# Kernel optimization log

Hardware: AMD Instinct MI355X
Metric: run time of the kernel (lower is better)

Reference implementation:

```python
import jax, jax.numpy as jnp
import numpy as np

B, C, L = 8, 2048, 256          # batch, seq (EEG channels), feature length
E = 3 * L                        # embed_dim = 768 (fused QKV width)
H = 4                            # attention heads
D = E // (3 * H)                 # head_dim = 64
SCALE = 8.0                      # hardcoded in the module (== sqrt(D) here)


def _layer_norm(x, gamma, beta, eps=1e-5):
    mu = jnp.mean(x, axis=-1, keepdims=True)
    var = jnp.var(x, axis=-1, keepdims=True)
    return (x - mu) * jax.lax.rsqrt(var + eps) * gamma + beta


def setup_inputs() -> dict:
    key = jax.random.key(0)
    ks = jax.random.split(key, 5)
    x = jax.random.normal(ks[0], (B, C, L), dtype=jnp.float32)
    # layers_1: Linear(L -> E) + LayerNorm(E)
    W1 = jax.random.normal(ks[1], (L, E), dtype=jnp.float32) / np.sqrt(L)
    b1 = jnp.zeros((E,), dtype=jnp.float32)
    g1 = jnp.ones((E,), dtype=jnp.float32)
    beta1 = jnp.zeros((E,), dtype=jnp.float32)
    # layers_2: Linear(L -> L) + LayerNorm(L)
    W2 = jax.random.normal(ks[2], (L, L), dtype=jnp.float32) / np.sqrt(L)
    b2 = jnp.zeros((L,), dtype=jnp.float32)
    g2 = jnp.ones((L,), dtype=jnp.float32)
    beta2 = jnp.zeros((L,), dtype=jnp.float32)
    return {"x": x, "W1": W1, "b1": b1, "g1": g1, "beta1": beta1,
            "W2": W2, "b2": b2, "g2": g2, "beta2": beta2}


def reference(x, W1, b1, g1, beta1, W2, b2, g2, beta2):
    b, c, _ = x.shape
    # layers_1 (dropout is identity in eval mode)
    y = _layer_norm(x @ W1 + b1, g1, beta1)                     # [b, c, E]
    qkv = y.reshape(b, c, 3, H, D).transpose(2, 0, 3, 1, 4)     # [3, b, H, c, D]
    q, k, v = qkv[0], qkv[1], qkv[2]
    attn = jax.nn.softmax(jnp.einsum('bhqd,bhkd->bhqk', q, k) / SCALE, axis=-1)
    o = jnp.einsum('bhqk,bhkd->bhqd', attn, v)                  # [b, H, c, D]
    o = o.transpose(0, 2, 1, 3).reshape(b, c, H * D)            # [b, c, L]
    # layers_2 + residual
    z = _layer_norm(o @ W2 + b2, g2, beta2) + x
    return z
```

## Files before the change

### kernel.cpp

```cpp
#include <hip/hip_runtime.h>
#include <hip/hip_bf16.h>

#define B_ 8
#define C_ 2048
#define L_ 256
#define E_ 768
#define H_ 4
#define D_ 64
#define M_ (B_*C_)

typedef __attribute__((ext_vector_type(8))) short short8v;
typedef __attribute__((ext_vector_type(4))) short short4v;
typedef __attribute__((ext_vector_type(4))) float f32x4;
typedef __attribute__((ext_vector_type(4))) unsigned uint4v;

__device__ __forceinline__ short f2bf(float f) {
  union { float f; unsigned u; } v; v.f = f;
  unsigned r = v.u + 0x7FFFu + ((v.u >> 16) & 1u);
  return (short)(r >> 16);
}
__device__ __forceinline__ unsigned cvtpk(float a, float b) {
  unsigned r;
  asm("v_cvt_pk_bf16_f32 %0, %1, %2" : "=v"(r) : "v"(a), "v"(b));
  return r;
}
__device__ __forceinline__ float exp2x(float x) {
  float r;
  asm("v_exp_f32 %0, %1" : "=v"(r) : "v"(x));
  return r;
}

__device__ __forceinline__ void gll16(const void* g, void* l) {
  __builtin_amdgcn_global_load_lds(
      (const __attribute__((address_space(1))) unsigned int*)g,
      (__attribute__((address_space(3))) unsigned int*)l, 16, 0, 0);
}

__global__ __launch_bounds__(256) void transpose_w_kernel(
    const float* __restrict__ W1, short* __restrict__ W1t,
    const float* __restrict__ W2, short* __restrict__ W2t) {
  __shared__ float ld[32][33];
  const int isW1 = blockIdx.y < 24;
  const float* W = isW1 ? W1 : W2;
  short* Wt = isW1 ? W1t : W2t;
  const int N = isW1 ? E_ : L_;
  const int k0 = blockIdx.x * 32, n0 = (isW1 ? blockIdx.y : blockIdx.y - 24) * 32;
  const int tx = threadIdx.x & 31, ty = threadIdx.x >> 5;
  #pragma unroll
  for (int j = 0; j < 4; ++j)
    ld[ty + j*8][tx] = W[(size_t)(k0 + ty + j*8) * N + n0 + tx];
  __syncthreads();
  const int r  = threadIdx.x >> 3;
  const int c0 = (threadIdx.x & 7) * 4;
  short4v o;
  o[0]=f2bf(ld[c0+0][r]); o[1]=f2bf(ld[c0+1][r]);
  o[2]=f2bf(ld[c0+2][r]); o[3]=f2bf(ld[c0+3][r]);
  *(short4v*)(Wt + (size_t)(n0 + r) * 256 + k0 + c0) = o;
}

__global__ __launch_bounds__(512, 2) void gemm1_ln_fused_kernel(
    const float* __restrict__ x, const short* __restrict__ W1t,
    const float* __restrict__ b1, const float* __restrict__ g1,
    const float* __restrict__ be1,
    short* __restrict__ Qg, short* __restrict__ Kg, short* __restrict__ Vtg) {
  __shared__ short As[32*264];
  __shared__ short tbuf[8][32][24];
  __shared__ float2 red[8][32];
  __shared__ float mu_s[32], rs_s[32];
  const int tid = threadIdx.x;
  const int w = tid >> 6, l = tid & 63, lo = l & 15, hi = l >> 4;
  const int m0 = blockIdx.x * 32;
  const int b = m0 >> 11, c0 = m0 & (C_ - 1);
  const int nbase = w * 96;

  {
    const int row = tid >> 4, cc = (tid & 15) * 16;
    const float* ap = x + (size_t)(m0 + row) * 256 + cc;
    float4 a0 = ((const float4*)ap)[0], a1 = ((const float4*)ap)[1];
    float4 a2 = ((const float4*)ap)[2], a3 = ((const float4*)ap)[3];
    uint4 p0, p1;
    p0.x = cvtpk(a0.x,a0.y); p0.y = cvtpk(a0.z,a0.w);
    p0.z = cvtpk(a1.x,a1.y); p0.w = cvtpk(a1.z,a1.w);
    p1.x = cvtpk(a2.x,a2.y); p1.y = cvtpk(a2.z,a2.w);
    p1.z = cvtpk(a3.x,a3.y); p1.w = cvtpk(a3.z,a3.w);
    *(uint4*)&As[row*264 + cc]     = p0;
    *(uint4*)&As[row*264 + cc + 8] = p1;
  }
  __syncthreads();

  f32x4 acc[2][6];
  #pragma unroll
  for (int m = 0; m < 2; ++m)
    #pragma unroll
    for (int n = 0; n < 6; ++n) acc[m][n] = (f32x4){0.f,0.f,0.f,0.f};

  const short* Wb = W1t + (size_t)(nbase + lo) * 256 + hi*8;
  short8v bf[6], bfN[6];
  #pragma unroll
  for (int n = 0; n < 6; ++n) bf[n] = *(const short8v*)(Wb + (size_t)(n*16) * 256);

  #pragma unroll
  for (int r8 = 0; r8 < 8; ++r8) {
    const int kof = r8 * 32;
    if (r8 < 7) {
      const int kofN = (r8 + 1) * 32;
      #pragma unroll
      for (int n = 0; n < 6; ++n)
        bfN[n] = *(const short8v*)(Wb + (size_t)(n*16) * 256 + kofN);
    }
    short8v af0 = *(short8v*)&As[lo*264      + kof + hi*8];
    short8v af1 = *(short8v*)&As[(16+lo)*264 + kof + hi*8];
    #pragma unroll
    for (int n = 0; n < 6; ++n) {
      acc[0][n] = __builtin_amdgcn_mfma_f32_16x16x32_bf16(af0, bf[n], acc[0][n], 0,0,0);
      acc[1][n] = __builtin_amdgcn_mfma_f32_16x16x32_bf16(af1, bf[n], acc[1][n], 0,0,0);
    }
    #pragma unroll
    for (int n = 0; n < 6; ++n) bf[n] = bfN[n];
  }

  float bb[6], ggv[6], eev[6];
  #pragma unroll
  for (int n = 0; n < 6; ++n) {
    int col = nbase + n*16 + lo;
    bb[n] = b1[col]; ggv[n] = g1[col]; eev[n] = be1[col];
  }
  #pragma unroll
  for (int m = 0; m < 2; ++m)
    #pragma unroll
    for (int r = 0; r < 4; ++r) {
      float s = 0.f, s2 = 0.f;
      #pragma unroll
      for (int n = 0; n < 6; ++n) {
        float v = acc[m][n][r] + bb[n];
        acc[m][n][r] = v;
        s += v; s2 += v*v;
      }
      #pragma unroll
      for (int off = 1; off < 16; off <<= 1) {
        s  += __shfl_xor(s, off);
        s2 += __shfl_xor(s2, off);
      }
      if (lo == 0) red[w][m*16 + hi*4 + r] = make_float2(s, s2);
    }
  __syncthreads();
  if (tid < 32) {
    float s = 0.f, s2 = 0.f;
    #pragma unroll
    for (int wv = 0; wv < 8; ++wv) { s += red[wv][tid].x; s2 += red[wv][tid].y; }
    float mu = s * (1.f / E_);
    float var = s2 * (1.f / E_) - mu * mu;
    mu_s[tid] = mu;
    rs_s[tid] = rsqrtf(var + 1e-5f);
  }
  __syncthreads();

  const float qs = 0.18033688011f;
  float muv[2][4], rsv[2][4];
  #pragma unroll
  for (int m = 0; m < 2; ++m)
    #pragma unroll
    for (int r = 0; r < 4; ++r) {
      int row = m*16 + hi*4 + r;
      muv[m][r] = mu_s[row]; rsv[m][r] = rs_s[row];
    }

  const int trow = l >> 1, tc = (l & 1) * 8;
  #pragma unroll
  for (int n = 0; n < 6; ++n) {
    const int e0b = nbase + n*16;
    if (e0b < 512) {
      const float qscale = (e0b < 256) ? qs : 1.f;
      #pragma unroll
      for (int m = 0; m < 2; ++m)
        #pragma unroll
        for (int r = 0; r < 4; ++r) {
          float v = (acc[m][n][r] - muv[m][r]) * rsv[m][r] * ggv[n] + eev[n];
          tbuf[w][m*16 + hi*4 + r][lo] = f2bf(v * qscale);
        }
      short8v tv = *(short8v*)&tbuf[w][trow][tc];
      const int c = c0 + trow;
      if (e0b < 256) {
        const int h = e0b >> 6, d0 = (e0b & 63) + tc;
        *(short8v*)(Qg + ((size_t)(b*H_ + h) * C_ + c) * D_ + d0) = tv;
      } else {
        const int eb = e0b - 256, h = eb >> 6, d0 = (eb & 63) + tc;
        int a5 = c & 31;
        int p5 = (((a5 >> 2) & 1) << 4) | (((a5 >> 3) & 3) << 2) | (a5 & 3);
        int cs = (c & ~31) | p5;
        *(short8v*)(Kg + ((size_t)(b*H_ + h) * C_ + cs) * D_
                      + (((d0 >> 3) ^ (cs & 7)) << 3)) = tv;
      }
    } else {
      const int e0 = e0b + lo;
      const int eb = e0 - 512, h = eb >> 6, d = eb & 63;
      #pragma unroll
      for (int m = 0; m < 2; ++m) {
        short4v pk;
        #pragma unroll
        for (int r = 0; r < 4; ++r)
          pk[r] = f2bf((acc[m][n][r] - muv[m][r]) * rsv[m][r] * ggv[n] + eev[n]);
        const int c = c0 + m*16 + hi*4;
        size_t off = ((size_t)(b*H_ + h) * D_ + d) * C_ + (c & ~63)
                   + ((((c & 63) >> 3) ^ (d & 7)) << 3) + (c & 7);
        *(short4v*)(Vtg + off) = pk;
      }
    }
  }
}

__global__ __launch_bounds__(512, 4) void attn_mfma_kernel(
    const short* __restrict__ Qg, const short* __restrict__ Kg,
    const short* __restrict__ Vtg, short* __restrict__ ob) {
  __shared__ short Ks[3][4096];
  __shared__ short Vs[3][4096];
  const int tid = threadIdx.x;
  const int w  = tid >> 6;
  const int l  = tid & 63, lo = l & 15, hi = l >> 4;
  const int sw = lo & 7;
  const int bh = blockIdx.x, qt = blockIdx.y;
  const size_t hd = (size_t)bh * (C_ * D_);
  const int q0 = qt * 128 + w * 16;

  const short8v bq0 = *(const short8v*)(Qg + hd + (size_t)(q0+lo)*D_ + hi*8);
  const short8v bq1 = *(const short8v*)(Qg + hd + (size_t)(q0+lo)*D_ + 32 + hi*8);

  short8v ones;
  #pragma unroll
  for (int j = 0; j < 8; ++j) ones[j] = (short)0x3F80;

  const short* Ktile = Kg + hd;
  const short* Vrow  = Vtg + hd;
  const int kOff = w*512 + l*8;
  const size_t vOff = (size_t)(w*8 + (l>>3)) * C_ + (l&7)*8;

  f32x4 Oacc[4] = {{0,0,0,0},{0,0,0,0},{0,0,0,0},{0,0,0,0}};
  f32x4 Lacc = {0.f, 0.f, 0.f, 0.f};
  const f32x4 zero4 = {0.f, 0.f, 0.f, 0.f};

  gll16(Ktile + kOff, &Ks[0][w*512]);
  gll16(Vrow + vOff,  &Vs[0][w*512]);

  int cur = 0, nxt = 1;
  for (int kt = 0; kt < 32; ++kt) {
    asm volatile("s_waitcnt vmcnt(0)" ::: "memory");
    __builtin_amdgcn_s_barrier();
    if (kt != 31) {
      const short* kn = Ktile + (size_t)(kt+1) * 4096;
      const short* vn = Vrow  + (size_t)(kt+1) * 64;
      gll16(kn + kOff, &Ks[nxt][w*512]);
      gll16(vn + vOff, &Vs[nxt][w*512]);
    }
    const short* Kc = &Ks[cur][0];
    const short* Vc = &Vs[cur][0];

    f32x4 st[4];
    __builtin_amdgcn_s_setprio(1);
    #pragma unroll
    for (int mt = 0; mt < 4; ++mt) {
      short8v ka = *(const short8v*)&Kc[(mt*16 + lo)*64 + ((hi ^ sw) << 3)];
      short8v kb = *(const short8v*)&Kc[(mt*16 + lo)*64 + (((4 + hi) ^ sw) << 3)];
      f32x4 z = __builtin_amdgcn_mfma_f32_16x16x32_bf16(ka, bq0, zero4, 0, 0, 0);
      st[mt]  = __builtin_amdgcn_mfma_f32_16x16x32_bf16(kb, bq1, z, 0, 0, 0);
    }
    __builtin_amdgcn_s_setprio(0);

    float ps[16];
    #pragma unroll
    for (int mt = 0; mt < 4; ++mt)
      #pragma unroll
      for (int r = 0; r < 4; ++r)
        ps[mt*4 + r] = exp2x(st[mt][r]);
    uint4v up0 = { cvtpk(ps[0], ps[1]),  cvtpk(ps[2], ps[3]),
                   cvtpk(ps[4], ps[5]),  cvtpk(ps[6], ps[7]) };
    uint4v up1 = { cvtpk(ps[8], ps[9]),  cvtpk(ps[10], ps[11]),
                   cvtpk(ps[12], ps[13]), cvtpk(ps[14], ps[15]) };
    short8v pa0 = __builtin_bit_cast(short8v, up0);
    short8v pa1 = __builtin_bit_cast(short8v, up1);

    __builtin_amdgcn_s_setprio(1);
    Lacc = __builtin_amdgcn_mfma_f32_16x16x32_bf16(pa0, ones, Lacc, 0, 0, 0);
    Lacc = __builtin_amdgcn_mfma_f32_16x16x32_bf16(pa1, ones, Lacc, 0, 0, 0);
    #pragma unroll
    for (int nt = 0; nt < 4; ++nt) {
      short8v vb0 = *(const short8v*)&Vc[(nt*16 + lo)*64 + ((hi ^ sw) << 3)];
      short8v vb1 = *(const short8v*)&Vc[(nt*16 + lo)*64 + (((4 + hi) ^ sw) << 3)];
      Oacc[nt] = __builtin_amdgcn_mfma_f32_16x16x32_bf16(pa0, vb0, Oacc[nt], 0,0,0);
      Oacc[nt] = __builtin_amdgcn_mfma_f32_16x16x32_bf16(pa1, vb1, Oacc[nt], 0,0,0);
    }
    __builtin_amdgcn_s_setprio(0);
    cur = nxt;
    nxt = (nxt == 2) ? 0 : nxt + 1;
  }

  float invL[4];
  #pragma unroll
  for (int r = 0; r < 4; ++r) invL[r] = 1.f / Lacc[r];
  const int b = bh >> 2, h = bh & 3;
  short* obp = ob + ((size_t)b * C_ + q0) * L_ + h * D_;
  #pragma unroll
  for (int nt = 0; nt < 4; ++nt)
    #pragma unroll
    for (int r = 0; r < 4; ++r)
      obp[(hi*4 + r) * L_ + nt*16 + lo] = f2bf(Oacc[nt][r] * invL[r]);
}

__global__ __launch_bounds__(256, 4) void gemm2_ln_mfma_kernel(
    const short* __restrict__ ob, const short* __restrict__ W2t,
    const float* __restrict__ b2, const float* __restrict__ g2,
    const float* __restrict__ be2, const float* __restrict__ x,
    float* __restrict__ out) {
  __shared__ short As[32*264];
  __shared__ float2 red[4][32];
  __shared__ float mu_s[32], rs_s[32];
  const int tid = threadIdx.x;
  const int w = tid >> 6, l = tid & 63, lo = l & 15, hi = l >> 4;
  const int m0 = blockIdx.x * 32;
  const int nbase = w * 64;

  #pragma unroll
  for (int i = 0; i < 4; ++i) {
    int id = tid + i * 256;
    int row = id >> 5, c8 = (id & 31) * 8;
    *(short8v*)&As[row*264 + c8] =
        *(const short8v*)(ob + (size_t)(m0 + row) * 256 + c8);
  }
  __syncthreads();

  f32x4 acc[2][4];
  #pragma unroll
  for (int m = 0; m < 2; ++m)
    #pragma unroll
    for (int n = 0; n < 4; ++n) acc[m][n] = (f32x4){0.f,0.f,0.f,0.f};

  #pragma unroll
  for (int kt = 0; kt < 4; ++kt)
    #pragma unroll
    for (int kk = 0; kk < 2; ++kk) {
      short8v bf[4];
      #pragma unroll
      for (int n = 0; n < 4; ++n)
        bf[n] = *(const short8v*)(W2t + (size_t)(nbase + n*16 + lo) * 256
                                     + kt*64 + kk*32 + hi*8);
      short8v af0 = *(short8v*)&As[lo*264      + kt*64 + kk*32 + hi*8];
      short8v af1 = *(short8v*)&As[(16+lo)*264 + kt*64 + kk*32 + hi*8];
      #pragma unroll
      for (int n = 0; n < 4; ++n) {
        acc[0][n] = __builtin_amdgcn_mfma_f32_16x16x32_bf16(af0, bf[n], acc[0][n], 0,0,0);
        acc[1][n] = __builtin_amdgcn_mfma_f32_16x16x32_bf16(af1, bf[n], acc[1][n], 0,0,0);
      }
    }

  float bb[4], gg[4], ee[4];
  #pragma unroll
  for (int n = 0; n < 4; ++n) {
    int col = nbase + n*16 + lo;
    bb[n] = b2[col]; gg[n] = g2[col]; ee[n] = be2[col];
  }
  #pragma unroll
  for (int m = 0; m < 2; ++m)
    #pragma unroll
    for (int r = 0; r < 4; ++r) {
      float s = 0.f, s2 = 0.f;
      #pragma unroll
      for (int n = 0; n < 4; ++n) {
        float v = acc[m][n][r] + bb[n];
        acc[m][n][r] = v;
        s += v; s2 += v*v;
      }
      #pragma unroll
      for (int off = 1; off < 16; off <<= 1) {
        s  += __shfl_xor(s, off);
        s2 += __shfl_xor(s2, off);
      }
      if (lo == 0) red[w][m*16 + hi*4 + r] = make_float2(s, s2);
    }
  __syncthreads();
  if (tid < 32) {
    float s = 0.f, s2 = 0.f;
    #pragma unroll
    for (int wv = 0; wv < 4; ++wv) { s += red[wv][tid].x; s2 += red[wv][tid].y; }
    float mu = s * (1.f / L_);
    float var = s2 * (1.f / L_) - mu * mu;
    mu_s[tid] = mu;
    rs_s[tid] = rsqrtf(var + 1e-5f);
  }
  __syncthreads();

  #pragma unroll
  for (int m = 0; m < 2; ++m) {
    float mu4[4], rs4[4];
    #pragma unroll
    for (int r = 0; r < 4; ++r) {
      int row = m*16 + hi*4 + r;
      mu4[r] = mu_s[row]; rs4[r] = rs_s[row];
    }
    #pragma unroll
    for (int r = 0; r < 4; ++r) {
      const int grow = m0 + m*16 + hi*4 + r;
      const float* xr = x + (size_t)grow * L_ + nbase;
      float* orow = out + (size_t)grow * L_ + nbase;
      #pragma unroll
      for (int n = 0; n < 4; ++n)
        orow[n*16 + lo] = (acc[m][n][r] - mu4[r]) * rs4[r] * gg[n] + ee[n]
                        + xr[n*16 + lo];
    }
  }
}

extern "C" void kernel_launch(void* const* d_in, const int* in_sizes, int n_in,
                              void* d_out, int out_size, void* d_ws, size_t ws_size,
                              hipStream_t stream) {
  const float* x   = (const float*)d_in[0];
  const float* W1  = (const float*)d_in[1];
  const float* b1  = (const float*)d_in[2];
  const float* g1  = (const float*)d_in[3];
  const float* be1 = (const float*)d_in[4];
  const float* W2  = (const float*)d_in[5];
  const float* b2  = (const float*)d_in[6];
  const float* g2  = (const float*)d_in[7];
  const float* be2 = (const float*)d_in[8];
  float* out = (float*)d_out;

  const size_t HDSZ = (size_t)B_ * H_ * C_ * D_;
  short* W1t = (short*)d_ws;
  short* W2t = W1t + (size_t)L_ * E_;
  short* Qg  = W2t + (size_t)L_ * L_;
  short* Kg  = Qg  + HDSZ;
  short* Vtg = Kg  + HDSZ;
  short* obm = Vtg + HDSZ;

  transpose_w_kernel<<<dim3(8, 32), 256, 0, stream>>>(W1, W1t, W2, W2t);
  gemm1_ln_fused_kernel<<<M_ / 32, 512, 0, stream>>>(x, W1t, b1, g1, be1, Qg, Kg, Vtg);
  attn_mfma_kernel<<<dim3(32, C_ / 128), 512, 0, stream>>>(Qg, Kg, Vtg, obm);
  gemm2_ln_mfma_kernel<<<M_ / 32, 256, 0, stream>>>(obm, W2t, b2, g2, be2, x, out);
}
```

Baseline: 98.12 us.

## Stage W1 tiles through swizzled LDS via direct global-to-LDS loads in GEMM1

Instead of each wave prefetching its W1 fragments from global memory into registers with double buffering, the block cooperatively loads each 768x32 bf16 K-slice of W1t into LDS using direct global-to-LDS loads. An XOR swizzle is applied to avoid bank conflicts, and the MFMA B operands are then read from LDS. This cuts register pressure and makes the global loads coalesced. In exchange it adds 48KB of LDS per block, which may hurt occupancy at 2 blocks/CU, plus two barriers per K step and a full vmcnt wait with no overlap of load and compute.

```diff
diff --git a/kernel.cpp b/kernel.cpp
--- a/kernel.cpp
+++ b/kernel.cpp
@@ -64,6 +64,7 @@
     const float* __restrict__ be1,
     short* __restrict__ Qg, short* __restrict__ Kg, short* __restrict__ Vtg) {
   __shared__ short As[32*264];
+  __shared__ short Bs[768*32];
   __shared__ short tbuf[8][32][24];
   __shared__ float2 red[8][32];
   __shared__ float mu_s[32], rs_s[32];
@@ -94,29 +95,29 @@
     #pragma unroll
     for (int n = 0; n < 6; ++n) acc[m][n] = (f32x4){0.f,0.f,0.f,0.f};
 
-  const short* Wb = W1t + (size_t)(nbase + lo) * 256 + hi*8;
-  short8v bf[6], bfN[6];
-  #pragma unroll
-  for (int n = 0; n < 6; ++n) bf[n] = *(const short8v*)(Wb + (size_t)(n*16) * 256);
-
-  #pragma unroll
+  const int srowl = l >> 2;
+  const int schunk = ((l & 3) ^ (srowl & 3)) << 3;
+
   for (int r8 = 0; r8 < 8; ++r8) {
-    const int kof = r8 * 32;
-    if (r8 < 7) {
-      const int kofN = (r8 + 1) * 32;
-      #pragma unroll
-      for (int n = 0; n < 6; ++n)
-        bfN[n] = *(const short8v*)(Wb + (size_t)(n*16) * 256 + kofN);
-    }
-    short8v af0 = *(short8v*)&As[lo*264      + kof + hi*8];
-    short8v af1 = *(short8v*)&As[(16+lo)*264 + kof + hi*8];
+    if (r8) __syncthreads();
+    #pragma unroll
+    for (int i = 0; i < 6; ++i) {
+      const short* src = W1t + (size_t)(i*128 + w*16 + srowl) * 256
+                       + r8*32 + schunk;
+      gll16(src, &Bs[i*4096 + w*512]);
+    }
+    asm volatile("s_waitcnt vmcnt(0)" ::: "memory");
+    __syncthreads();
+
+    short8v af0 = *(short8v*)&As[lo*264      + r8*32 + hi*8];
+    short8v af1 = *(short8v*)&As[(16+lo)*264 + r8*32 + hi*8];
     #pragma unroll
     for (int n = 0; n < 6; ++n) {
-      acc[0][n] = __builtin_amdgcn_mfma_f32_16x16x32_bf16(af0, bf[n], acc[0][n], 0,0,0);
-      acc[1][n] = __builtin_amdgcn_mfma_f32_16x16x32_bf16(af1, bf[n], acc[1][n], 0,0,0);
-    }
-    #pragma unroll
-    for (int n = 0; n < 6; ++n) bf[n] = bfN[n];
+      const int row = nbase + n*16 + lo;
+      short8v bfn = *(short8v*)&Bs[row*32 + ((hi ^ (lo & 3)) << 3)];
+      acc[0][n] = __builtin_amdgcn_mfma_f32_16x16x32_bf16(af0, bfn, acc[0][n], 0,0,0);
+      acc[1][n] = __builtin_amdgcn_mfma_f32_16x16x32_bf16(af1, bfn, acc[1][n], 0,0,0);
+    }
   }
 
   float bb[6], ggv[6], eev[6];
```

Result: faster. 94.98 us (-3.2%).
